# Performance work log

Hardware: AMD Instinct MI355X
Metric: run time of the kernel (lower is better)

## Reference

```python
import jax, jax.numpy as jnp
import numpy as np

N, E, F_IN, HID, HEADS, NCLS = 50000, 800000, 500, 16, 8, 40
NEG_SLOPE = 0.2


def setup_inputs() -> dict:
    key = jax.random.key(0)
    ks = jax.random.split(key, 10)
    x = jax.random.normal(ks[0], (N, F_IN), jnp.float32)
    edge_index = jax.random.randint(ks[1], (2, E), 0, N)
    W1 = jax.random.normal(ks[2], (F_IN, HEADS * HID), jnp.float32) * (1.0 / np.sqrt(F_IN))
    a_src1 = jax.random.normal(ks[3], (HEADS, HID), jnp.float32) * 0.1
    a_dst1 = jax.random.normal(ks[4], (HEADS, HID), jnp.float32) * 0.1
    b1 = jnp.zeros((HEADS * HID,), jnp.float32)
    W2 = jax.random.normal(ks[5], (HEADS * HID, NCLS), jnp.float32) * (1.0 / np.sqrt(HEADS * HID))
    a_src2 = jax.random.normal(ks[6], (1, NCLS), jnp.float32) * 0.1
    a_dst2 = jax.random.normal(ks[7], (1, NCLS), jnp.float32) * 0.1
    b2 = jnp.zeros((NCLS,), jnp.float32)
    return {"x": x, "edge_index": edge_index, "W1": W1, "a_src1": a_src1,
            "a_dst1": a_dst1, "b1": b1, "W2": W2, "a_src2": a_src2,
            "a_dst2": a_dst2, "b2": b2}


def gat_layer(x, edge_index, W, a_src, a_dst, b, heads, ch, concat):
    n = x.shape[0]
    h = (x @ W).reshape(n, heads, ch)                 # [N,H,C]
    alpha_src = jnp.sum(h * a_src, axis=-1)           # [N,H]
    alpha_dst = jnp.sum(h * a_dst, axis=-1)           # [N,H]
    loop = jnp.arange(n)                              # PyG add_self_loops=True
    src = jnp.concatenate([edge_index[0], loop])
    dst = jnp.concatenate([edge_index[1], loop])
    e = jax.nn.leaky_relu(alpha_src[src] + alpha_dst[dst], NEG_SLOPE)  # [E',H]
    # segment softmax over destination nodes
    m = jax.ops.segment_max(e, dst, num_segments=n)
    ex = jnp.exp(e - m[dst])
    denom = jax.ops.segment_sum(ex, dst, num_segments=n)
    alpha = ex / (denom[dst] + 1e-16)                 # [E',H]
    out = jax.ops.segment_sum(h[src] * alpha[:, :, None], dst, num_segments=n)  # [N,H,C]
    out = out.reshape(n, heads * ch) if concat else out.mean(axis=1)
    return out + b


def reference(x, edge_index, W1, a_src1, a_dst1, b1, W2, a_src2, a_dst2, b2):
    h = jax.nn.elu(gat_layer(x, edge_index, W1, a_src1, a_dst1, b1, HEADS, HID, True))
    # dropout p=0.6 is identity in eval mode
    h = gat_layer(h, edge_index, W2, a_src2, a_dst2, b2, 1, NCLS, False)
    return jax.nn.log_softmax(h, axis=1)
```

## Files before the change

kernel.cpp:

```cpp
#include <hip/hip_runtime.h>
#include <hip/hip_bf16.h>
#include <math.h>

#define N_NODES 50000
#define F_IN    500
#define HEADS   8
#define HID     16
#define HH      128
#define NCLS    40
#define NEG     0.2f

typedef _Float16 f16x2 __attribute__((ext_vector_type(2)));
typedef _Float16 f16x4 __attribute__((ext_vector_type(4)));
typedef _Float16 f16x8 __attribute__((ext_vector_type(8)));
typedef float    f32x4 __attribute__((ext_vector_type(4)));

__device__ __forceinline__ float lrelu(float x) { return x >= 0.f ? x : NEG * x; }

__global__ void convW_kernel(const float* __restrict__ W1, _Float16* __restrict__ Wt) {
    int i = blockIdx.x * 256 + threadIdx.x;
    if (i >= 128 * 512) return;
    int c = i >> 9, k = i & 511;
    Wt[i] = (k < F_IN) ? (_Float16)W1[k * HH + c] : (_Float16)0.f;
}

#define KT   128
#define LDP  136
__global__ __launch_bounds__(256) void gemm1_mfma(const float* __restrict__ x,
                                                  const _Float16* __restrict__ Wt,
                                                  _Float16* __restrict__ h1h) {
    __shared__ _Float16 As[64 * LDP];
    __shared__ _Float16 Bs[128 * LDP];
    const int t = threadIdx.x;
    const int lane = t & 63, w = t >> 6;
    const int rowBase = blockIdx.x * 64;

    f32x4 acc[8];
#pragma unroll
    for (int n = 0; n < 8; ++n) acc[n] = (f32x4){0.f, 0.f, 0.f, 0.f};

    const int fa = t & 31, ra = t >> 5;
    const int gb = t & 15, cb = t >> 4;

    for (int kt = 0; kt < 4; ++kt) {
        const int kt0 = kt * KT;
#pragma unroll
        for (int p = 0; p < 8; ++p) {
            int row = ra + 8 * p;
            int grow = rowBase + row;
            int k0 = kt0 + 4 * fa;
            float4 v = make_float4(0.f, 0.f, 0.f, 0.f);
            if (grow < N_NODES && k0 < F_IN)
                v = *(const float4*)&x[(size_t)grow * F_IN + k0];
            f16x4 hv = {(_Float16)v.x, (_Float16)v.y, (_Float16)v.z, (_Float16)v.w};
            *(f16x4*)&As[row * LDP + 4 * fa] = hv;
        }
#pragma unroll
        for (int p = 0; p < 8; ++p) {
            int c = cb + 16 * p;
            *(f16x8*)&Bs[c * LDP + 8 * gb] = *(const f16x8*)&Wt[c * 512 + kt0 + 8 * gb];
        }
        __syncthreads();
#pragma unroll
        for (int ks = 0; ks < 4; ++ks) {
            int kk = ks * 32 + (lane >> 4) * 8;
            f16x8 a = *(const f16x8*)&As[(16 * w + (lane & 15)) * LDP + kk];
#pragma unroll
            for (int n = 0; n < 8; ++n) {
                f16x8 b = *(const f16x8*)&Bs[(16 * n + (lane & 15)) * LDP + kk];
                acc[n] = __builtin_amdgcn_mfma_f32_16x16x32_f16(a, b, acc[n], 0, 0, 0);
            }
        }
        __syncthreads();
    }
    const int colb = lane & 15, rq = lane >> 4;
#pragma unroll
    for (int n = 0; n < 8; ++n) {
#pragma unroll
        for (int r = 0; r < 4; ++r) {
            int grow = rowBase + 16 * w + rq * 4 + r;
            if (grow < N_NODES) h1h[(size_t)grow * HH + 16 * n + colb] = (_Float16)acc[n][r];
        }
    }
}

__global__ void alpha1_kernel(const _Float16* __restrict__ h1h,
                              const float* __restrict__ a_src,
                              const float* __restrict__ a_dst,
                              float* __restrict__ asrc, float* __restrict__ adst) {
    int idx = blockIdx.x * blockDim.x + threadIdx.x;
    if (idx >= N_NODES * HEADS) return;
    int n = idx >> 3, h = idx & 7;
    const f16x8* hp = (const f16x8*)&h1h[(size_t)n * HH + h * HID];
    float s = 0.f, d = 0.f;
#pragma unroll
    for (int c = 0; c < 2; ++c) {
        f16x8 hv = hp[c];
#pragma unroll
        for (int i = 0; i < 8; ++i) {
            float f = (float)hv[i];
            s += f * a_src[h * HID + c * 8 + i];
            d += f * a_dst[h * HID + c * 8 + i];
        }
    }
    asrc[idx] = s;
    adst[idx] = d;
}

__global__ void zero_int_kernel(int* __restrict__ p, int n) {
    int i = blockIdx.x * blockDim.x + threadIdx.x;
    if (i < n) p[i] = 0;
}

__global__ void count_kernel(const int* __restrict__ ei, int* __restrict__ deg,
                             int E, int EP) {
    int e = blockIdx.x * blockDim.x + threadIdx.x;
    if (e >= EP) return;
    int dst = (e < E) ? ei[E + e] : (e - E);
    atomicAdd(&deg[dst], 1);
}

__global__ __launch_bounds__(256) void scan1_kernel(const int* __restrict__ deg,
                                                    int* __restrict__ offs,
                                                    int* __restrict__ bsums, int n) {
    __shared__ int sm[256];
    int tid = threadIdx.x, i = blockIdx.x * 256 + tid;
    int v = (i < n) ? deg[i] : 0;
    sm[tid] = v;
    __syncthreads();
    for (int off = 1; off < 256; off <<= 1) {
        int t = 0;
        if (tid >= off) t = sm[tid - off];
        __syncthreads();
        if (tid >= off) sm[tid] += t;
        __syncthreads();
    }
    if (i < n) offs[i] = sm[tid] - v;
    if (tid == 255) bsums[blockIdx.x] = sm[255];
}

__global__ __launch_bounds__(256) void scan2_kernel(const int* __restrict__ bsums,
                                                    int* __restrict__ boffs, int nb,
                                                    int* __restrict__ offs, int n) {
    __shared__ int sm[256];
    int tid = threadIdx.x;
    int v = (tid < nb) ? bsums[tid] : 0;
    sm[tid] = v;
    __syncthreads();
    for (int off = 1; off < 256; off <<= 1) {
        int t = 0;
        if (tid >= off) t = sm[tid - off];
        __syncthreads();
        if (tid >= off) sm[tid] += t;
        __syncthreads();
    }
    if (tid < nb) boffs[tid] = sm[tid] - v;
    if (tid == 255) offs[n] = sm[255];
}

__global__ __launch_bounds__(256) void scan3_kernel(int* __restrict__ offs,
                                                    int* __restrict__ cursor,
                                                    const int* __restrict__ boffs, int n) {
    int i = blockIdx.x * 256 + threadIdx.x;
    if (i >= n) return;
    int o = offs[i] + boffs[blockIdx.x];
    offs[i] = o;
    cursor[i] = o;
}

__global__ void fill_kernel(const int* __restrict__ ei, int* __restrict__ cursor,
                            int* __restrict__ bsrc, int E, int EP) {
    int e = blockIdx.x * blockDim.x + threadIdx.x;
    if (e >= EP) return;
    int src, dst;
    if (e < E) { src = ei[e]; dst = ei[E + e]; }
    else       { src = e - E; dst = e - E; }
    int slot = atomicAdd(&cursor[dst], 1);
    bsrc[slot] = src;
}

__global__ __launch_bounds__(256) void agg1_kernel(const _Float16* __restrict__ h1h,
                                                   const float* __restrict__ asrc,
                                                   const float* __restrict__ adst,
                                                   const int* __restrict__ offs,
                                                   const int* __restrict__ bsrc,
                                                   const float* __restrict__ b1,
                                                   _Float16* __restrict__ h1bh) {
    int lane = threadIdx.x & 63;
    int node = blockIdx.x * 4 + (threadIdx.x >> 6);
    if (node >= N_NODES) return;
    int beg = offs[node], end = offs[node + 1];
    int hh = lane >> 3;
    float adv = adst[node * 8 + hh];

    float acc0 = 0.f, acc1 = 0.f, dsum = 0.f;
    int j = beg;
    for (; j + 2 <= end; j += 2) {
        int s0 = bsrc[j], s1 = bsrc[j + 1];
        float sa0 = asrc[s0 * 8 + hh];
        float sa1 = asrc[s1 * 8 + hh];
        f16x2 hv0 = *(const f16x2*)&h1h[(size_t)s0 * HH + 2 * lane];
        f16x2 hv1 = *(const f16x2*)&h1h[(size_t)s1 * HH + 2 * lane];
        float w0 = __expf(lrelu(sa0 + adv));
        float w1 = __expf(lrelu(sa1 + adv));
        dsum += w0 + w1;
        acc0 += w0 * (float)hv0[0] + w1 * (float)hv1[0];
        acc1 += w0 * (float)hv0[1] + w1 * (float)hv1[1];
    }
    if (j < end) {
        int s0 = bsrc[j];
        float sa0 = asrc[s0 * 8 + hh];
        f16x2 hv0 = *(const f16x2*)&h1h[(size_t)s0 * HH + 2 * lane];
        float w0 = __expf(lrelu(sa0 + adv));
        dsum += w0;
        acc0 += w0 * (float)hv0[0];
        acc1 += w0 * (float)hv0[1];
    }
    float rv = 1.f / (dsum + 1e-16f);
    float2 bv = *(const float2*)&b1[2 * lane];
    float v0 = acc0 * rv + bv.x;
    float v1 = acc1 * rv + bv.y;
    v0 = v0 > 0.f ? v0 : __expf(v0) - 1.f;
    v1 = v1 > 0.f ? v1 : __expf(v1) - 1.f;
    f16x2 o = {(_Float16)v0, (_Float16)v1};
    *(f16x2*)&h1bh[(size_t)node * HH + 2 * lane] = o;
}

__global__ __launch_bounds__(256) void gemm2_kernel(const _Float16* __restrict__ h1bh,
                                                    const float* __restrict__ W2,
                                                    _Float16* __restrict__ h2h) {
    __shared__ float Ws[HH * NCLS];
    for (int i = threadIdx.x; i < HH * NCLS; i += 256) Ws[i] = W2[i];
    __syncthreads();
    int idx = blockIdx.x * 256 + threadIdx.x;
    if (idx >= N_NODES * NCLS) return;
    int n = idx / NCLS, c = idx - n * NCLS;
    const f16x8* hp = (const f16x8*)&h1bh[(size_t)n * HH];
    float acc = 0.f;
#pragma unroll
    for (int k8 = 0; k8 < HH / 8; ++k8) {
        f16x8 hv = hp[k8];
#pragma unroll
        for (int i = 0; i < 8; ++i)
            acc += (float)hv[i] * Ws[(k8 * 8 + i) * NCLS + c];
    }
    h2h[idx] = (_Float16)acc;
}

__global__ void alpha2_kernel(const _Float16* __restrict__ h2h,
                              const float* __restrict__ a_src,
                              const float* __restrict__ a_dst,
                              float* __restrict__ asrc, float* __restrict__ adst) {
    int n = blockIdx.x * blockDim.x + threadIdx.x;
    if (n >= N_NODES) return;
    const f16x8* hp = (const f16x8*)&h2h[(size_t)n * NCLS];
    float s = 0.f, d = 0.f;
#pragma unroll
    for (int c8 = 0; c8 < NCLS / 8; ++c8) {
        f16x8 hv = hp[c8];
#pragma unroll
        for (int i = 0; i < 8; ++i) {
            float f = (float)hv[i];
            s += f * a_src[c8 * 8 + i];
            d += f * a_dst[c8 * 8 + i];
        }
    }
    asrc[n] = s;
    adst[n] = d;
}

__global__ __launch_bounds__(256) void agg2_kernel(const _Float16* __restrict__ h2h,
                                                   const float* __restrict__ asrc,
                                                   const float* __restrict__ adst,
                                                   const int* __restrict__ offs,
                                                   const int* __restrict__ bsrc,
                                                   const float* __restrict__ b2,
                                                   float* __restrict__ out) {
    int lane = threadIdx.x & 63;
    int node = blockIdx.x * 4 + (threadIdx.x >> 6);
    if (node >= N_NODES) return;
    int beg = offs[node], end = offs[node + 1];
    float adv = adst[node];
    bool act = lane < NCLS / 2;

    float acc0 = 0.f, acc1 = 0.f, dsum = 0.f;
    int j = beg;
    for (; j + 2 <= end; j += 2) {
        int s0 = bsrc[j], s1 = bsrc[j + 1];
        float w0 = __expf(lrelu(asrc[s0] + adv));
        float w1 = __expf(lrelu(asrc[s1] + adv));
        f16x2 hv0 = {(_Float16)0.f, (_Float16)0.f}, hv1 = hv0;
        if (act) {
            hv0 = *(const f16x2*)&h2h[(size_t)s0 * NCLS + 2 * lane];
            hv1 = *(const f16x2*)&h2h[(size_t)s1 * NCLS + 2 * lane];
        }
        dsum += w0 + w1;
        acc0 += w0 * (float)hv0[0] + w1 * (float)hv1[0];
        acc1 += w0 * (float)hv0[1] + w1 * (float)hv1[1];
    }
    if (j < end) {
        int s0 = bsrc[j];
        float w0 = __expf(lrelu(asrc[s0] + adv));
        f16x2 hv0 = {(_Float16)0.f, (_Float16)0.f};
        if (act) hv0 = *(const f16x2*)&h2h[(size_t)s0 * NCLS + 2 * lane];
        dsum += w0;
        acc0 += w0 * (float)hv0[0];
        acc1 += w0 * (float)hv0[1];
    }
    float rd = 1.f / (dsum + 1e-16f);
    float v0 = -1e30f, v1 = -1e30f;
    if (act) {
        float2 bv = *(const float2*)&b2[2 * lane];
        v0 = acc0 * rd + bv.x;
        v1 = acc1 * rd + bv.y;
    }
    float m = fmaxf(v0, v1);
#pragma unroll
    for (int o = 32; o; o >>= 1) m = fmaxf(m, __shfl_xor(m, o, 64));
    float p = act ? (__expf(v0 - m) + __expf(v1 - m)) : 0.f;
#pragma unroll
    for (int o = 32; o; o >>= 1) p += __shfl_xor(p, o, 64);
    float ls = m + __logf(p);
    if (act) {
        float2 ov = make_float2(v0 - ls, v1 - ls);
        *(float2*)&out[(size_t)node * NCLS + 2 * lane] = ov;
    }
}

extern "C" void kernel_launch(void* const* d_in, const int* in_sizes, int n_in,
                              void* d_out, int out_size, void* d_ws, size_t ws_size,
                              hipStream_t stream) {
    const float* x      = (const float*)d_in[0];
    const int*   ei     = (const int*)d_in[1];
    const float* W1     = (const float*)d_in[2];
    const float* a_src1 = (const float*)d_in[3];
    const float* a_dst1 = (const float*)d_in[4];
    const float* b1     = (const float*)d_in[5];
    const float* W2     = (const float*)d_in[6];
    const float* a_src2 = (const float*)d_in[7];
    const float* a_dst2 = (const float*)d_in[8];
    const float* b2     = (const float*)d_in[9];
    float* out = (float*)d_out;

    const int E  = in_sizes[1] / 2;
    const int EP = E + N_NODES;
    const int NB = (N_NODES + 255) / 256;

    char* w = (char*)d_ws;
    _Float16* h1h   = (_Float16*)(w + 0);
    _Float16* h1bh  = (_Float16*)(w + 12800000);
    float*    asrc1 = (float*)(w + 25600000);
    float*    adst1 = (float*)(w + 27200000);
    _Float16* h2h   = (_Float16*)(w + 28800000);
    float*    asrc2 = (float*)(w + 32800000);
    float*    adst2 = (float*)(w + 33000000);
    int*      deg   = (int*)(w + 33200000);
    int*      offs  = (int*)(w + 33400064);
    int*      cursor= (int*)(w + 33600128);
    int*      bsrc  = (int*)(w + 33800192);
    _Float16* Wt    = (_Float16*)(w + 37200256);
    int*      bsums = (int*)(w + 37331328);
    int*      boffs = (int*)(w + 37332352);

    zero_int_kernel<<<(N_NODES + 255) / 256, 256, 0, stream>>>(deg, N_NODES);
    convW_kernel<<<(128 * 512 + 255) / 256, 256, 0, stream>>>(W1, Wt);
    gemm1_mfma<<<(N_NODES + 63) / 64, 256, 0, stream>>>(x, Wt, h1h);
    alpha1_kernel<<<(N_NODES * HEADS + 255) / 256, 256, 0, stream>>>(h1h, a_src1, a_dst1,
                                                                     asrc1, adst1);
    count_kernel<<<(EP + 255) / 256, 256, 0, stream>>>(ei, deg, E, EP);
    scan1_kernel<<<NB, 256, 0, stream>>>(deg, offs, bsums, N_NODES);
    scan2_kernel<<<1, 256, 0, stream>>>(bsums, boffs, NB, offs, N_NODES);
    scan3_kernel<<<NB, 256, 0, stream>>>(offs, cursor, boffs, N_NODES);
    fill_kernel<<<(EP + 255) / 256, 256, 0, stream>>>(ei, cursor, bsrc, E, EP);
    agg1_kernel<<<(N_NODES + 3) / 4, 256, 0, stream>>>(h1h, asrc1, adst1, offs, bsrc, b1, h1bh);
    gemm2_kernel<<<(N_NODES * NCLS + 255) / 256, 256, 0, stream>>>(h1bh, W2, h2h);
    alpha2_kernel<<<(N_NODES + 255) / 256, 256, 0, stream>>>(h2h, a_src2, a_dst2,
                                                             asrc2, adst2);
    agg2_kernel<<<(N_NODES + 3) / 4, 256, 0, stream>>>(h2h, asrc2, adst2, offs, bsrc, b2, out);
}
```

Before: 446.7 us.

## Load GEMM A fragments directly into registers with next-tile prefetch

The x operand of the first GEMM no longer goes through shared memory. Each lane loads its own MFMA A-fragment straight from global memory into registers, converts it to fp16, and issues the loads for the next K tile before the current MFMAs run. This drops the As LDS staging and its reads, and overlaps the global x loads with compute. In exchange it uses more registers, and the global reads are less coalesced because each lane reads 32-byte pieces of separate rows.

Result: no change. 442.5 us (-0.9%).

```diff
diff --git a/kernel.cpp b/kernel.cpp
--- a/kernel.cpp
+++ b/kernel.cpp
@@ -24,51 +24,62 @@
     Wt[i] = (k < F_IN) ? (_Float16)W1[k * HH + c] : (_Float16)0.f;
 }
 
-#define KT   128
-#define LDP  136
+#define LDPB 136
 __global__ __launch_bounds__(256) void gemm1_mfma(const float* __restrict__ x,
                                                   const _Float16* __restrict__ Wt,
                                                   _Float16* __restrict__ h1h) {
-    __shared__ _Float16 As[64 * LDP];
-    __shared__ _Float16 Bs[128 * LDP];
+    __shared__ _Float16 Bs[128 * LDPB];
     const int t = threadIdx.x;
     const int lane = t & 63, w = t >> 6;
     const int rowBase = blockIdx.x * 64;
+    const int arow = rowBase + 16 * w + (lane & 15);
+    const bool rowok = arow < N_NODES;
+    const int klo = (lane >> 4) * 8;
+    const float* xrow = x + (size_t)arow * F_IN;
 
     f32x4 acc[8];
 #pragma unroll
     for (int n = 0; n < 8; ++n) acc[n] = (f32x4){0.f, 0.f, 0.f, 0.f};
 
-    const int fa = t & 31, ra = t >> 5;
     const int gb = t & 15, cb = t >> 4;
 
+    float4 pa0[4], pa1[4];
+#pragma unroll
+    for (int ks = 0; ks < 4; ++ks) {
+        int kk = ks * 32 + klo;
+        pa0[ks] = (rowok && kk < F_IN)     ? *(const float4*)&xrow[kk]     : make_float4(0, 0, 0, 0);
+        pa1[ks] = (rowok && kk + 4 < F_IN) ? *(const float4*)&xrow[kk + 4] : make_float4(0, 0, 0, 0);
+    }
+
     for (int kt = 0; kt < 4; ++kt) {
-        const int kt0 = kt * KT;
-#pragma unroll
-        for (int p = 0; p < 8; ++p) {
-            int row = ra + 8 * p;
-            int grow = rowBase + row;
-            int k0 = kt0 + 4 * fa;
-            float4 v = make_float4(0.f, 0.f, 0.f, 0.f);
-            if (grow < N_NODES && k0 < F_IN)
-                v = *(const float4*)&x[(size_t)grow * F_IN + k0];
-            f16x4 hv = {(_Float16)v.x, (_Float16)v.y, (_Float16)v.z, (_Float16)v.w};
-            *(f16x4*)&As[row * LDP + 4 * fa] = hv;
-        }
 #pragma unroll
         for (int p = 0; p < 8; ++p) {
             int c = cb + 16 * p;
-            *(f16x8*)&Bs[c * LDP + 8 * gb] = *(const f16x8*)&Wt[c * 512 + kt0 + 8 * gb];
-        }
-        __syncthreads();
+            *(f16x8*)&Bs[c * LDPB + 8 * gb] = *(const f16x8*)&Wt[c * 512 + kt * 128 + 8 * gb];
+        }
+        __syncthreads();
+
+        f16x8 afr[4];
 #pragma unroll
         for (int ks = 0; ks < 4; ++ks) {
-            int kk = ks * 32 + (lane >> 4) * 8;
-            f16x8 a = *(const f16x8*)&As[(16 * w + (lane & 15)) * LDP + kk];
+            float4 a0 = pa0[ks], a1 = pa1[ks];
+            afr[ks] = (f16x8){(_Float16)a0.x, (_Float16)a0.y, (_Float16)a0.z, (_Float16)a0.w,
+                              (_Float16)a1.x, (_Float16)a1.y, (_Float16)a1.z, (_Float16)a1.w};
+        }
+        if (kt < 3) {
+#pragma unroll
+            for (int ks = 0; ks < 4; ++ks) {
+                int kk = (kt + 1) * 128 + ks * 32 + klo;
+                pa0[ks] = (rowok && kk < F_IN)     ? *(const float4*)&xrow[kk]     : make_float4(0, 0, 0, 0);
+                pa1[ks] = (rowok && kk + 4 < F_IN) ? *(const float4*)&xrow[kk + 4] : make_float4(0, 0, 0, 0);
+            }
+        }
+#pragma unroll
+        for (int ks = 0; ks < 4; ++ks) {
 #pragma unroll
             for (int n = 0; n < 8; ++n) {
-                f16x8 b = *(const f16x8*)&Bs[(16 * n + (lane & 15)) * LDP + kk];
-                acc[n] = __builtin_amdgcn_mfma_f32_16x16x32_f16(a, b, acc[n], 0, 0, 0);
+                f16x8 b = *(const f16x8*)&Bs[(16 * n + (lane & 15)) * LDPB + ks * 32 + klo];
+                acc[n] = __builtin_amdgcn_mfma_f32_16x16x32_f16(afr[ks], b, acc[n], 0, 0, 0);
             }
         }
         __syncthreads();
```
